# Kernel tuning notes

Hardware: AMD Instinct MI355X
Metric: run time of the kernel (lower is better)

## Reference

```python
import jax, jax.numpy as jnp
import numpy as np

LMAX = 5
RESOLUTION = 12
ASPECT_RATIO = 2
BATCH = 256
NB = 2 * RESOLUTION                       # res_beta = 24
NA = round(2 * ASPECT_RATIO * RESOLUTION)  # res_alpha = res_gamma = 48
DIM = sum((2 * l + 1) ** 2 for l in range(LMAX + 1))  # 286

# normalize2mom constant for tanh: (E_{z~N(0,1)}[tanh(z)^2])^{-1/2}
_x = np.linspace(-12.0, 12.0, 1_000_001)
_pdf = np.exp(-0.5 * _x * _x) / np.sqrt(2.0 * np.pi)
ACT_CST = float(np.trapz(np.tanh(_x) ** 2 * _pdf, _x) ** -0.5)  # ~1.5927


def _su2_generators(j):
    m = np.arange(-j, j)
    raising = np.diag(-np.sqrt(j * (j + 1) - m * (m + 1)), k=-1).astype(complex)
    m = np.arange(-j + 1, j + 1)
    lowering = np.diag(np.sqrt(j * (j + 1) - m * (m - 1)), k=1).astype(complex)
    m = np.arange(-j, j + 1)
    return np.stack([0.5 * (raising + lowering), np.diag(1j * m), -0.5j * (raising - lowering)])


def _q_real_to_complex(l):
    q = np.zeros((2 * l + 1, 2 * l + 1), dtype=complex)
    for m in range(-l, 0):
        q[l + m, l + abs(m)] = 1 / np.sqrt(2)
        q[l + m, l - abs(m)] = -1j / np.sqrt(2)
    q[l, l] = 1
    for m in range(1, l + 1):
        q[l + m, l + abs(m)] = (-1) ** m / np.sqrt(2)
        q[l + m, l - abs(m)] = 1j * (-1) ** m / np.sqrt(2)
    return (-1j) ** l * q


def _so3_generators(l):
    X = _su2_generators(l)
    Q = _q_real_to_complex(l)
    return np.real(np.conj(Q.T)[None] @ X @ Q[None])  # real [3, 2l+1, 2l+1]


def _expm_angles(A, t):
    """exp(t_n * A) for real antisymmetric A via eigendecomposition. -> [n, d, d] real"""
    vals, vecs = np.linalg.eig(A.astype(complex))
    inv = np.linalg.inv(vecs)
    phases = np.exp(t[:, None] * vals[None, :])  # [n, d]
    return np.real(np.einsum('ij,nj,jk->nik', vecs, phases, inv))


def _build_D_and_qw():
    # Euler angle grids (e3nn SO3Grid convention)
    b = (np.arange(NB) + 0.5) / NB * np.pi          # beta   [nb]
    a = np.arange(NA) / NA * 2.0 * np.pi            # alpha=gamma [na]
    blocks = []
    for l in range(LMAX + 1):
        X = _so3_generators(l)
        Ra = _expm_angles(X[1], a)   # exp(alpha * X1)  [na,d,d]
        Rb = _expm_angles(X[0], b)   # exp(beta  * X0)  [nb,d,d]
        # D^l(a,b,c) = Ra[a] @ Rb[b] @ Ra[c]
        Dl = np.einsum('xij,yjk,zkl->xyzil', Ra, Rb, Ra)
        blocks.append(np.sqrt(2 * l + 1) * Dl.reshape(NA, NB, NA, -1))
    D = np.concatenate(blocks, axis=-1).astype(np.float32)  # [na, nb, na, dim]
    # lie_learn / Kostelec-Rockmore quadrature weights for beta
    bb = NB // 2
    k = np.arange(bb)
    j = np.arange(2 * bb)
    w = (2.0 / bb) * np.sin(np.pi * (2 * j + 1) / (4.0 * bb)) * np.sum(
        (1.0 / (2 * k + 1))[None, :]
        * np.sin((2 * j[:, None] + 1) * (2 * k[None, :] + 1) * np.pi / (4.0 * bb)),
        axis=1,
    )
    w = w / (2.0 * (2 * bb) ** 2)
    qw = (w * NB ** 2 / NA ** 2).astype(np.float32)  # [nb]
    return jnp.asarray(D), jnp.asarray(qw)


def setup_inputs() -> dict:
    key = jax.random.key(0)
    features = jax.random.normal(key, (BATCH, DIM), dtype=jnp.float32)
    D, qw = _build_D_and_qw()
    return {"features": features, "D": D, "qw": qw}


def reference(features, D, qw):
    dim = D.shape[-1]
    s = jnp.sqrt(jnp.asarray(dim, features.dtype))
    # to_grid: [B, dim] x [na, nb, na, dim] -> [B, na, nb, na]
    g = jnp.einsum('bi,xyzi->bxyz', features, D) / s
    # normalized pointwise nonlinearity on SO(3) samples
    g = ACT_CST * jnp.tanh(g)
    # from_grid: quadrature-weighted projection back onto flat Wigner basis
    return jnp.einsum('bxyz,y,xyzi->bi', g, qw, D) * s
```

## Files before the change

kernel.cpp:

```cpp
#include <hip/hip_runtime.h>
#include <hip/hip_bf16.h>

#define DIM    286
#define DIMP   288
#define NZTOT  55296
#define NBATCH 256
#define NB_    24
#define NA_    48
#define ZC     32
#define NTILES 1728
#define NCHUNK 256
#define S_CONST 16.911534525287763f
#define INV_S   0.05913123959890826f
#define ACT_CST 1.5927f
#define TWO_LOG2E 2.8853900817779268f

typedef short bf16x8 __attribute__((ext_vector_type(8)));
typedef float f32x4  __attribute__((ext_vector_type(4)));

#define WS_FBF  0u
#define WS_DBF  147456u
#define WS_DT   (WS_DBF + 31850496u)
#define WS_PART (WS_DT + 31850496u)

typedef const __attribute__((address_space(1))) char GA;
typedef __attribute__((address_space(3))) char LA;
__device__ __forceinline__ void gload_lds16(const void* g, void* l) {
    __builtin_amdgcn_global_load_lds((GA*)g, (LA*)l, 16, 0, 0);
}

__global__ void k_prep(const float* __restrict__ F, const float* __restrict__ D,
                       const float* __restrict__ qw,
                       __hip_bfloat16* __restrict__ Fbf,
                       __hip_bfloat16* __restrict__ Dbf, __hip_bfloat16* __restrict__ Dt2) {
    __shared__ __align__(16) float T[9152];
    __shared__ float qs[24];
    int t = threadIdx.x;
    int bid = blockIdx.x;
    if (bid >= NTILES) {
        int o = (bid - NTILES) * 256 + t;
        int row = o / DIMP, col = o % DIMP;
        float v = (col < DIM) ? F[row * DIM + col] * INV_S : 0.f;
        Fbf[o] = __float2bfloat16(v);
        return;
    }
    int z0 = bid * 32;
    if (t < 24) qs[t] = qw[t] * S_CONST;
    {
        int wave = t >> 6, lane = t & 63;
        const char* src = (const char*)(D + (size_t)z0 * DIM);
        char* dst = (char*)T;
        #pragma unroll
        for (int j = 0; j < 9; ++j) {
            int c = wave + j * 4;
            if (c < 35 || (c == 35 && lane < 48))
                gload_lds16(src + c * 1024 + lane * 16, dst + c * 1024);
        }
    }
    asm volatile("s_waitcnt vmcnt(0)" ::: "memory");
    __syncthreads();
    char* dbB = (char*)Dbf + (size_t)bid * 18432;
    for (int m = 0; m < 18; ++m) {
        int d = t + m * 256;
        int z = d / 144, i2 = d % 144;
        int i = i2 * 2;
        __hip_bfloat162 o2;
        if (i < DIM) {
            float2 v = *(const float2*)(&T[z * DIM + i]);
            o2.x = __float2bfloat16(v.x); o2.y = __float2bfloat16(v.y);
        } else {
            o2.x = __float2bfloat16(0.f); o2.y = o2.x;
        }
        int off = (((i >> 5) * 2048) + z * 64 + (i & 31) * 2) ^ ((z & 7) << 4);
        *(__hip_bfloat162*)(dbB + off) = o2;
    }
    char* dtB = (char*)Dt2 + (size_t)bid * 18432;
    for (int s = 0; s < 5; ++s) {
        int idx = t + s * 256;
        if (idx < 1152) {
            int i = idx >> 2, zc = idx & 3;
            __hip_bfloat16 o8[8];
            #pragma unroll
            for (int j = 0; j < 8; ++j) {
                int zl = zc * 8 + j;
                int y = ((z0 + zl) / NA_) % NB_;
                o8[j] = __float2bfloat16(T[zl * DIM + i] * qs[y]);
            }
            int off = (i * 64 + zc * 16) ^ ((i & 7) << 4);
            *(bf16x8*)(dtB + off) = *(const bf16x8*)o8;
        }
    }
}

__launch_bounds__(256, 2)
__global__ void k_main(const __hip_bfloat16* __restrict__ Fbf,
                       const __hip_bfloat16* __restrict__ Dbf,
                       const __hip_bfloat16* __restrict__ Dt2,
                       __hip_bfloat16* __restrict__ part) {
    __shared__ __align__(16) char DsB[18432];
    __shared__ __align__(16) char DtB[18432];
    __shared__ __align__(16) char GsB[8192];

    int t = threadIdx.x;
    int wave = t >> 6, lane = t & 63, ln = lane & 15, q = lane >> 4;
    int xsw = (ln & 7) << 4;
    int cA = (ln * 64 + q * 16) ^ xsw;

    bf16x8 fa[2][9];
    int rowbase = blockIdx.y * 128 + wave * 32;
    #pragma unroll
    for (int h = 0; h < 2; ++h) {
        const __hip_bfloat16* fp = Fbf + (size_t)(rowbase + h * 16 + ln) * DIMP + q * 8;
        #pragma unroll
        for (int ks = 0; ks < 9; ++ks) fa[h][ks] = *(const bf16x8*)(fp + ks * 32);
    }

    f32x4 acc[2][18];
    #pragma unroll
    for (int h = 0; h < 2; ++h)
        #pragma unroll
        for (int n = 0; n < 18; ++n) acc[h][n] = (f32x4){0.f, 0.f, 0.f, 0.f};

    int bx = blockIdx.x;
    int tstart = (bx < 192) ? bx * 7 : bx * 6 + 192;
    int ntile = (bx < 192) ? 7 : 6;

    #pragma unroll 1
    for (int k = 0; k < ntile; ++k) {
        int tz = tstart + k;
        {
            const char* src; char* dst;
            if (wave < 2) {
                src = (const char*)Dbf + (size_t)tz * 18432 + wave * 9216 + lane * 16;
                dst = DsB + wave * 9216;
            } else {
                src = (const char*)Dt2 + (size_t)tz * 18432 + (wave - 2) * 9216 + lane * 16;
                dst = DtB + (wave - 2) * 9216;
            }
            #pragma unroll
            for (int j = 0; j < 9; ++j)
                gload_lds16(src + j * 1024, dst + j * 1024);
        }
        asm volatile("s_waitcnt vmcnt(0)" ::: "memory");
        __syncthreads();
        f32x4 g00 = (f32x4){0.f,0.f,0.f,0.f}, g01 = (f32x4){0.f,0.f,0.f,0.f};
        f32x4 g10 = (f32x4){0.f,0.f,0.f,0.f}, g11 = (f32x4){0.f,0.f,0.f,0.f};
        #pragma unroll
        for (int ks = 0; ks < 9; ++ks) {
            bf16x8 b0 = *(const bf16x8*)(DsB + ks * 2048 + cA);
            bf16x8 b1 = *(const bf16x8*)(DsB + ks * 2048 + 1024 + cA);
            g00 = __builtin_amdgcn_mfma_f32_16x16x32_bf16(fa[0][ks], b0, g00, 0, 0, 0);
            g01 = __builtin_amdgcn_mfma_f32_16x16x32_bf16(fa[0][ks], b1, g01, 0, 0, 0);
            g10 = __builtin_amdgcn_mfma_f32_16x16x32_bf16(fa[1][ks], b0, g10, 0, 0, 0);
            g11 = __builtin_amdgcn_mfma_f32_16x16x32_bf16(fa[1][ks], b1, g11, 0, 0, 0);
        }
        #pragma unroll
        for (int h = 0; h < 2; ++h) {
            #pragma unroll
            for (int zh = 0; zh < 2; ++zh) {
                f32x4 g = (h == 0) ? (zh == 0 ? g00 : g01) : (zh == 0 ? g10 : g11);
                #pragma unroll
                for (int r = 0; r < 4; ++r) {
                    float x = g[r];
                    float a = fabsf(x);
                    float e = __builtin_amdgcn_exp2f(-TWO_LOG2E * a);
                    float v = ACT_CST - 2.f * ACT_CST * e * __builtin_amdgcn_rcpf(1.f + e);
                    v = copysignf(v, x);
                    int row = h * 16 + q * 4 + r;
                    int goff = (wave << 11) + ((row * 64 + (zh * 16 + ln) * 2) ^ ((row & 7) << 4));
                    *(__hip_bfloat16*)(GsB + goff) = __float2bfloat16(v);
                }
            }
        }
        bf16x8 a20 = *(const bf16x8*)(GsB + (wave << 11) + cA);
        bf16x8 a21 = *(const bf16x8*)(GsB + (wave << 11) + 1024 + cA);
        #pragma unroll
        for (int nf = 0; nf < 18; ++nf) {
            bf16x8 b2 = *(const bf16x8*)(DtB + nf * 1024 + cA);
            acc[0][nf] = __builtin_amdgcn_mfma_f32_16x16x32_bf16(a20, b2, acc[0][nf], 0, 0, 0);
            acc[1][nf] = __builtin_amdgcn_mfma_f32_16x16x32_bf16(a21, b2, acc[1][nf], 0, 0, 0);
        }
        __syncthreads();
    }
    __hip_bfloat16* pw = part + (size_t)blockIdx.x * (NBATCH * DIMP)
                       + ((size_t)blockIdx.y * 128 + wave * 32) * DIMP;
    #pragma unroll
    for (int h = 0; h < 2; ++h) {
        #pragma unroll
        for (int m = 0; m < 9; ++m) {
            __hip_bfloat16 o8[8];
            #pragma unroll
            for (int j = 0; j < 8; ++j)
                o8[j] = __float2bfloat16(acc[h][2 * m + (j >> 2)][j & 3]);
            *(bf16x8*)(pw + (size_t)((h * 9 + m) * 64 + lane) * 8) = *(const bf16x8*)o8;
        }
    }
}

__global__ void k_reduce(const __hip_bfloat16* __restrict__ part, float* __restrict__ out) {
    __shared__ float red[3][16][8];
    int t = threadIdx.x, wave = t >> 6, lane = t & 63;
    int j = lane & 15;
    int zg = wave * 4 + (lane >> 4);
    int s = blockIdx.x * 16 + j;
    const __hip_bfloat16* p = part + (size_t)s * 8;
    float sum[8];
    #pragma unroll
    for (int kk = 0; kk < 8; ++kk) sum[kk] = 0.f;
    #pragma unroll 4
    for (int ii = 0; ii < 16; ++ii) {
        bf16x8 v = *(const bf16x8*)(p + (size_t)(zg * 16 + ii) * (NBATCH * DIMP));
        #pragma unroll
        for (int kk = 0; kk < 8; ++kk) {
            __hip_bfloat16 h; *(short*)&h = v[kk];
            sum[kk] += __bfloat162float(h);
        }
    }
    #pragma unroll
    for (int kk = 0; kk < 8; ++kk) {
        sum[kk] += __shfl_down(sum[kk], 16);
        sum[kk] += __shfl_down(sum[kk], 32);
    }
    if (wave > 0 && lane < 16) {
        #pragma unroll
        for (int kk = 0; kk < 8; ++kk) red[wave - 1][lane][kk] = sum[kk];
    }
    __syncthreads();
    if (wave == 0 && lane < 16) {
        #pragma unroll
        for (int w = 0; w < 3; ++w)
            #pragma unroll
            for (int kk = 0; kk < 8; ++kk) sum[kk] += red[w][lane][kk];
        int wr = s / 1152, si = s % 1152;
        int lane_m = si % 64, m9 = si / 64;
        int h = m9 / 9, m = m9 % 9, q = lane_m >> 4, ln = lane_m & 15;
        int rowb = wr * 32 + h * 16 + q * 4;
        #pragma unroll
        for (int j8 = 0; j8 < 8; ++j8) {
            int nf = 2 * m + (j8 >> 2), r = j8 & 3;
            int i = nf * 16 + ln;
            if (i < DIM) out[(rowb + r) * DIM + i] = sum[j8];
        }
    }
}

extern "C" void kernel_launch(void* const* d_in, const int* in_sizes, int n_in,
                              void* d_out, int out_size, void* d_ws, size_t ws_size,
                              hipStream_t stream) {
    const float* F  = (const float*)d_in[0];
    const float* D  = (const float*)d_in[1];
    const float* qw = (const float*)d_in[2];
    char* ws = (char*)d_ws;
    __hip_bfloat16* Fbf = (__hip_bfloat16*)(ws + WS_FBF);
    __hip_bfloat16* Dbf = (__hip_bfloat16*)(ws + WS_DBF);
    __hip_bfloat16* Dt2 = (__hip_bfloat16*)(ws + WS_DT);
    __hip_bfloat16* part = (__hip_bfloat16*)(ws + WS_PART);

    k_prep<<<NTILES + 288, 256, 0, stream>>>(F, D, qw, Fbf, Dbf, Dt2);
    k_main<<<dim3(NCHUNK, 2), 256, 0, stream>>>(Fbf, Dbf, Dt2, part);
    k_reduce<<<576, 256, 0, stream>>>(part, (float*)d_out);
}
```

Baseline: 151.4 us.

## Double-buffer interleaved D tiles and merge batch halves into 512-thread blocks

Prep now writes D and weighted D^T tiles interleaved into one contiguous 36 KB tile. The main kernel uses 512-thread blocks covering all 256 batch rows, so each D tile is loaded once per block instead of twice across blockIdx.y. It also double-buffers the tiles in LDS, prefetching the next tile while computing the current one. LDS per block grows to about 88 KB, which may limit occupancy, and each thread block has fewer blocks to schedule.

```diff
diff --git a/kernel.cpp b/kernel.cpp
--- a/kernel.cpp
+++ b/kernel.cpp
@@ -3,7 +3,6 @@
 
 #define DIM    286
 #define DIMP   288
-#define NZTOT  55296
 #define NBATCH 256
 #define NB_    24
 #define NA_    48
@@ -18,10 +17,11 @@
 typedef short bf16x8 __attribute__((ext_vector_type(8)));
 typedef float f32x4  __attribute__((ext_vector_type(4)));
 
+#define TILE_B 36864u
+
 #define WS_FBF  0u
-#define WS_DBF  147456u
-#define WS_DT   (WS_DBF + 31850496u)
-#define WS_PART (WS_DT + 31850496u)
+#define WS_DT   147456u
+#define WS_PART (WS_DT + 63700992u)
 
 typedef const __attribute__((address_space(1))) char GA;
 typedef __attribute__((address_space(3))) char LA;
@@ -31,8 +31,7 @@
 
 __global__ void k_prep(const float* __restrict__ F, const float* __restrict__ D,
                        const float* __restrict__ qw,
-                       __hip_bfloat16* __restrict__ Fbf,
-                       __hip_bfloat16* __restrict__ Dbf, __hip_bfloat16* __restrict__ Dt2) {
+                       __hip_bfloat16* __restrict__ Fbf, char* __restrict__ DT) {
     __shared__ __align__(16) float T[9152];
     __shared__ float qs[24];
     int t = threadIdx.x;
@@ -59,7 +58,7 @@
     }
     asm volatile("s_waitcnt vmcnt(0)" ::: "memory");
     __syncthreads();
-    char* dbB = (char*)Dbf + (size_t)bid * 18432;
+    char* tb = DT + (size_t)bid * TILE_B;
     for (int m = 0; m < 18; ++m) {
         int d = t + m * 256;
         int z = d / 144, i2 = d % 144;
@@ -72,9 +71,8 @@
             o2.x = __float2bfloat16(0.f); o2.y = o2.x;
         }
         int off = (((i >> 5) * 2048) + z * 64 + (i & 31) * 2) ^ ((z & 7) << 4);
-        *(__hip_bfloat162*)(dbB + off) = o2;
-    }
-    char* dtB = (char*)Dt2 + (size_t)bid * 18432;
+        *(__hip_bfloat162*)(tb + off) = o2;
+    }
     for (int s = 0; s < 5; ++s) {
         int idx = t + s * 256;
         if (idx < 1152) {
@@ -87,27 +85,24 @@
                 o8[j] = __float2bfloat16(T[zl * DIM + i] * qs[y]);
             }
             int off = (i * 64 + zc * 16) ^ ((i & 7) << 4);
-            *(bf16x8*)(dtB + off) = *(const bf16x8*)o8;
-        }
-    }
-}
-
-__launch_bounds__(256, 2)
+            *(bf16x8*)(tb + 18432 + off) = *(const bf16x8*)o8;
+        }
+    }
+}
+
+__launch_bounds__(512, 2)
 __global__ void k_main(const __hip_bfloat16* __restrict__ Fbf,
-                       const __hip_bfloat16* __restrict__ Dbf,
-                       const __hip_bfloat16* __restrict__ Dt2,
+                       const char* __restrict__ DT,
                        __hip_bfloat16* __restrict__ part) {
-    __shared__ __align__(16) char DsB[18432];
-    __shared__ __align__(16) char DtB[18432];
-    __shared__ __align__(16) char GsB[8192];
+    __shared__ __align__(16) char SB[2][36864];
+    __shared__ __align__(16) char GsB[16384];
 
     int t = threadIdx.x;
     int wave = t >> 6, lane = t & 63, ln = lane & 15, q = lane >> 4;
-    int xsw = (ln & 7) << 4;
-    int cA = (ln * 64 + q * 16) ^ xsw;
+    int cA = (ln * 64 + q * 16) ^ ((ln & 7) << 4);
 
     bf16x8 fa[2][9];
-    int rowbase = blockIdx.y * 128 + wave * 32;
+    int rowbase = wave * 32;
     #pragma unroll
     for (int h = 0; h < 2; ++h) {
         const __hip_bfloat16* fp = Fbf + (size_t)(rowbase + h * 16 + ln) * DIMP + q * 8;
@@ -125,30 +120,35 @@
     int tstart = (bx < 192) ? bx * 7 : bx * 6 + 192;
     int ntile = (bx < 192) ? 7 : 6;
 
+    const char* srcT = DT + (size_t)tstart * TILE_B;
+    int lo16 = lane * 16;
+
+    #pragma unroll
+    for (int j = 0; j < 5; ++j) {
+        int c = wave + j * 8;
+        if (c < 36) gload_lds16(srcT + c * 1024 + lo16, SB[0] + c * 1024);
+    }
+    asm volatile("s_waitcnt vmcnt(0)" ::: "memory");
+    __syncthreads();
+
     #pragma unroll 1
     for (int k = 0; k < ntile; ++k) {
-        int tz = tstart + k;
-        {
-            const char* src; char* dst;
-            if (wave < 2) {
-                src = (const char*)Dbf + (size_t)tz * 18432 + wave * 9216 + lane * 16;
-                dst = DsB + wave * 9216;
-            } else {
-                src = (const char*)Dt2 + (size_t)tz * 18432 + (wave - 2) * 9216 + lane * 16;
-                dst = DtB + (wave - 2) * 9216;
+        const char* cb = SB[k & 1];
+        if (k + 1 < ntile) {
+            const char* s2 = srcT + (size_t)(k + 1) * TILE_B;
+            char* d2 = SB[(k + 1) & 1];
+            #pragma unroll
+            for (int j = 0; j < 5; ++j) {
+                int c = wave + j * 8;
+                if (c < 36) gload_lds16(s2 + c * 1024 + lo16, d2 + c * 1024);
             }
-            #pragma unroll
-            for (int j = 0; j < 9; ++j)
-                gload_lds16(src + j * 1024, dst + j * 1024);
-        }
-        asm volatile("s_waitcnt vmcnt(0)" ::: "memory");
-        __syncthreads();
+        }
         f32x4 g00 = (f32x4){0.f,0.f,0.f,0.f}, g01 = (f32x4){0.f,0.f,0.f,0.f};
         f32x4 g10 = (f32x4){0.f,0.f,0.f,0.f}, g11 = (f32x4){0.f,0.f,0.f,0.f};
         #pragma unroll
         for (int ks = 0; ks < 9; ++ks) {
-            bf16x8 b0 = *(const bf16x8*)(DsB + ks * 2048 + cA);
-            bf16x8 b1 = *(const bf16x8*)(DsB + ks * 2048 + 1024 + cA);
+            bf16x8 b0 = *(const bf16x8*)(cb + ks * 2048 + cA);
+            bf16x8 b1 = *(const bf16x8*)(cb + ks * 2048 + 1024 + cA);
             g00 = __builtin_amdgcn_mfma_f32_16x16x32_bf16(fa[0][ks], b0, g00, 0, 0, 0);
             g01 = __builtin_amdgcn_mfma_f32_16x16x32_bf16(fa[0][ks], b1, g01, 0, 0, 0);
             g10 = __builtin_amdgcn_mfma_f32_16x16x32_bf16(fa[1][ks], b0, g10, 0, 0, 0);
@@ -176,14 +176,14 @@
         bf16x8 a21 = *(const bf16x8*)(GsB + (wave << 11) + 1024 + cA);
         #pragma unroll
         for (int nf = 0; nf < 18; ++nf) {
-            bf16x8 b2 = *(const bf16x8*)(DtB + nf * 1024 + cA);
+            bf16x8 b2 = *(const bf16x8*)(cb + 18432 + nf * 1024 + cA);
             acc[0][nf] = __builtin_amdgcn_mfma_f32_16x16x32_bf16(a20, b2, acc[0][nf], 0, 0, 0);
             acc[1][nf] = __builtin_amdgcn_mfma_f32_16x16x32_bf16(a21, b2, acc[1][nf], 0, 0, 0);
         }
+        asm volatile("s_waitcnt vmcnt(0)" ::: "memory");
         __syncthreads();
     }
-    __hip_bfloat16* pw = part + (size_t)blockIdx.x * (NBATCH * DIMP)
-                       + ((size_t)blockIdx.y * 128 + wave * 32) * DIMP;
+    __hip_bfloat16* pw = part + (size_t)bx * (NBATCH * DIMP) + (size_t)rowbase * DIMP;
     #pragma unroll
     for (int h = 0; h < 2; ++h) {
         #pragma unroll
@@ -252,11 +252,10 @@
     const float* qw = (const float*)d_in[2];
     char* ws = (char*)d_ws;
     __hip_bfloat16* Fbf = (__hip_bfloat16*)(ws + WS_FBF);
-    __hip_bfloat16* Dbf = (__hip_bfloat16*)(ws + WS_DBF);
-    __hip_bfloat16* Dt2 = (__hip_bfloat16*)(ws + WS_DT);
+    char* DT = ws + WS_DT;
     __hip_bfloat16* part = (__hip_bfloat16*)(ws + WS_PART);
 
-    k_prep<<<NTILES + 288, 256, 0, stream>>>(F, D, qw, Fbf, Dbf, Dt2);
-    k_main<<<dim3(NCHUNK, 2), 256, 0, stream>>>(Fbf, Dbf, Dt2, part);
+    k_prep<<<NTILES + 288, 256, 0, stream>>>(F, D, qw, Fbf, DT);
+    k_main<<<NCHUNK, 512, 0, stream>>>(Fbf, DT, part);
     k_reduce<<<576, 256, 0, stream>>>(part, (float*)d_out);
 }
```

Measured after the change: 153.5 us. No clear change (+1.4%).
